# Kernel optimization log

Measured on AMD Instinct MI355X. Metric: run time of the kernel, lower is better.

Reference implementation:

```python
import jax, jax.numpy as jnp
import numpy as np
from jax.ops import segment_sum

N_NODES = 100000

def gcn_conv(x, ei, W, b, n):
    # PyG GCNConv: add self-loops, symmetric deg^-1/2 normalization,
    # linear transform (no lin bias), scatter-sum at target, then conv bias.
    src = jnp.concatenate([ei[0], jnp.arange(n)])  # [E+N]
    dst = jnp.concatenate([ei[1], jnp.arange(n)])
    deg = segment_sum(jnp.ones_like(dst, dtype=x.dtype), dst, num_segments=n)
    dinv = jnp.where(deg > 0, jax.lax.rsqrt(deg), 0.0)
    norm = dinv[src] * dinv[dst]                   # [E+N]
    h = x @ W.T                                    # [N, out] transform before gather
    msg = h[src] * norm[:, None]                   # [E+N, out]
    return segment_sum(msg, dst, num_segments=n) + b

def sage_conv_mean(x, ei, Wl, bl, Wr, n):
    # PyG SAGEConv(aggr='mean'): out = lin_l(mean_{j->i} x_j) + lin_r(x_i)
    src, dst = ei[0], ei[1]
    s = segment_sum(x[src], dst, num_segments=n)   # [N, d]
    cnt = segment_sum(jnp.ones_like(dst, dtype=x.dtype), dst, num_segments=n)
    mean = s / jnp.maximum(cnt, 1.0)[:, None]
    return mean @ Wl.T + bl + x @ Wr.T

def setup_inputs() -> dict:
    key = jax.random.key(0)
    k1, k2, k3, k4, k5, k6 = jax.random.split(key, 6)
    in_dim, hid = 128, 128
    n, e = N_NODES, 1600000
    feat = jax.random.normal(k1, (n, in_dim), dtype=jnp.float32)
    ei = jax.random.randint(k2, (2, e), 0, n, dtype=jnp.int64)
    W1 = jax.random.normal(k3, (hid, in_dim), dtype=jnp.float32) * 0.05
    b1 = jnp.zeros((hid,), dtype=jnp.float32)
    Wl = jax.random.normal(k4, (hid, hid), dtype=jnp.float32) * 0.05
    bl = jnp.zeros((hid,), dtype=jnp.float32)
    Wr = jax.random.normal(k5, (hid, hid), dtype=jnp.float32) * 0.05
    return {"feat": feat, "ei": ei, "W1": W1, "b1": b1, "Wl": Wl, "bl": bl, "Wr": Wr}

def reference(feat, ei, W1, b1, Wl, bl, Wr):
    n = feat.shape[0]
    h = jax.nn.relu(gcn_conv(feat, ei, W1, b1, n))
    h = jax.nn.relu(sage_conv_mean(h, ei, Wl, bl, Wr, n))
    return h
```

## Files before the change

### kernel.cpp

```cpp
#include <hip/hip_runtime.h>

typedef unsigned int uint;
typedef unsigned short ushort;
typedef short sv8 __attribute__((ext_vector_type(8)));
typedef float f32x4 __attribute__((ext_vector_type(4)));
typedef ushort u16x8 __attribute__((ext_vector_type(8)));

__device__ __forceinline__ ushort f2b(float f) {
  uint u = __float_as_uint(f);
  return (ushort)((u + 0x7FFFu + ((u >> 16) & 1u)) >> 16);
}
__device__ __forceinline__ float b2f_lo(uint p) { return __uint_as_float(p << 16); }
__device__ __forceinline__ float b2f_hi(uint p) { return __uint_as_float(p & 0xFFFF0000u); }
__device__ __forceinline__ uint cvtpk(float lo, float hi) {
  uint r;
  asm("v_cvt_pk_bf16_f32 %0, %1, %2" : "=v"(r) : "v"(lo), "v"(hi));
  return r;
}

#define MFMA16(acc, a, b) \
  asm volatile("v_mfma_f32_16x16x32_bf16 %0, %1, %2, %0" : "+v"(acc) : "v"(a), "v"(b))
#define DOT2(acc, p, d) \
  asm("v_dot2_f32_bf16 %0, %1, %2, %0" : "+v"(acc) : "v"(p), "v"(d))

#define GATHER16(SRC, jj)                                                     \
  {                                                                           \
    uint pa = (uint)__shfl((int)packed, (jj) + q);                            \
    uint pb = (uint)__shfl((int)packed, (jj) + 4 + q);                        \
    uint pc = (uint)__shfl((int)packed, (jj) + 8 + q);                        \
    uint pd = (uint)__shfl((int)packed, (jj) + 12 + q);                       \
    uint4 va = *(const uint4*)&SRC[(size_t)(pa & 0x1FFFFu) * 128 + lc * 8];   \
    uint4 vb = *(const uint4*)&SRC[(size_t)(pb & 0x1FFFFu) * 128 + lc * 8];   \
    uint4 vc = *(const uint4*)&SRC[(size_t)(pc & 0x1FFFFu) * 128 + lc * 8];   \
    uint4 vd = *(const uint4*)&SRC[(size_t)(pd & 0x1FFFFu) * 128 + lc * 8];   \
    uint dab = (pa >> 17) | ((pb >> 17) << 16);                               \
    uint dcd = (pc >> 17) | ((pd >> 17) << 16);                               \
    uint p;                                                                   \
    p = __builtin_amdgcn_perm(va.x, vb.x, 0x01000504u); DOT2(acc[0], p, dab); \
    p = __builtin_amdgcn_perm(va.x, vb.x, 0x03020706u); DOT2(acc[1], p, dab); \
    p = __builtin_amdgcn_perm(va.y, vb.y, 0x01000504u); DOT2(acc[2], p, dab); \
    p = __builtin_amdgcn_perm(va.y, vb.y, 0x03020706u); DOT2(acc[3], p, dab); \
    p = __builtin_amdgcn_perm(va.z, vb.z, 0x01000504u); DOT2(acc[4], p, dab); \
    p = __builtin_amdgcn_perm(va.z, vb.z, 0x03020706u); DOT2(acc[5], p, dab); \
    p = __builtin_amdgcn_perm(va.w, vb.w, 0x01000504u); DOT2(acc[6], p, dab); \
    p = __builtin_amdgcn_perm(va.w, vb.w, 0x03020706u); DOT2(acc[7], p, dab); \
    p = __builtin_amdgcn_perm(vc.x, vd.x, 0x01000504u); DOT2(acc[0], p, dcd); \
    p = __builtin_amdgcn_perm(vc.x, vd.x, 0x03020706u); DOT2(acc[1], p, dcd); \
    p = __builtin_amdgcn_perm(vc.y, vd.y, 0x01000504u); DOT2(acc[2], p, dcd); \
    p = __builtin_amdgcn_perm(vc.y, vd.y, 0x03020706u); DOT2(acc[3], p, dcd); \
    p = __builtin_amdgcn_perm(vc.z, vd.z, 0x01000504u); DOT2(acc[4], p, dcd); \
    p = __builtin_amdgcn_perm(vc.z, vd.z, 0x03020706u); DOT2(acc[5], p, dcd); \
    p = __builtin_amdgcn_perm(vc.w, vd.w, 0x01000504u); DOT2(acc[6], p, dcd); \
    p = __builtin_amdgcn_perm(vc.w, vd.w, 0x03020706u); DOT2(acc[7], p, dcd); \
  }


__global__ __launch_bounds__(256) void k_hist1(const int* __restrict__ dst,
                                               int* __restrict__ counts, int E) {
  __shared__ int h[256];
  int t = threadIdx.x;
  h[t] = 0;
  __syncthreads();
#pragma unroll
  for (int i = 0; i < 16; ++i) {
    int idx = blockIdx.x * 16384 + i * 1024 + t * 4;
    if (idx + 4 <= E) {
      int4 d = *(const int4*)&dst[idx];
      atomicAdd(&h[d.x >> 10], 1);
      atomicAdd(&h[d.y >> 10], 1);
      atomicAdd(&h[d.z >> 10], 1);
      atomicAdd(&h[d.w >> 10], 1);
    } else {
      for (int k = 0; k < 4; ++k)
        if (idx + k < E) atomicAdd(&h[dst[idx + k] >> 10], 1);
    }
  }
  __syncthreads();
  counts[blockIdx.x * 256 + t] = h[t];
}

__global__ __launch_bounds__(256) void k_colscan(int* __restrict__ counts,
                                                 int* __restrict__ bbase,
                                                 int* __restrict__ btot,
                                                 int* __restrict__ rowptr,
                                                 int NBLK, int N, int E) {
  __shared__ int s[256];
  int b = threadIdx.x;
  int run = 0;
#pragma unroll 4
  for (int blk = 0; blk < NBLK; ++blk) {
    int v = counts[blk * 256 + b];
    counts[blk * 256 + b] = run;
    run += v;
  }
  s[b] = run;
  __syncthreads();
  int incl = run;
  for (int off = 1; off < 256; off <<= 1) {
    int u = (b >= off) ? s[b - off] : 0;
    __syncthreads();
    s[b] += u;
    __syncthreads();
  }
  incl = s[b];
  bbase[b] = incl - run;
  btot[b] = run;
  if (b == 0) rowptr[N] = E;
}

__global__ __launch_bounds__(256) void k_scatter(const int* __restrict__ ei,
                                                 const int* __restrict__ counts,
                                                 const int* __restrict__ bbase,
                                                 uint* __restrict__ keyval, int E) {
  __shared__ int h[256];
  __shared__ int base[256];
  int t = threadIdx.x;
  base[t] = bbase[t] + counts[blockIdx.x * 256 + t];
  h[t] = 0;
  __syncthreads();
#pragma unroll
  for (int i = 0; i < 16; ++i) {
    int idx = blockIdx.x * 16384 + i * 1024 + t * 4;
    if (idx + 4 <= E) {
      int4 sv = *(const int4*)&ei[idx];
      int4 dv = *(const int4*)&ei[E + idx];
      int b0 = dv.x >> 10, b1 = dv.y >> 10, b2 = dv.z >> 10, b3 = dv.w >> 10;
      int r0 = atomicAdd(&h[b0], 1);
      keyval[base[b0] + r0] = (uint)sv.x | (((uint)dv.x & 1023u) << 17);
      int r1 = atomicAdd(&h[b1], 1);
      keyval[base[b1] + r1] = (uint)sv.y | (((uint)dv.y & 1023u) << 17);
      int r2 = atomicAdd(&h[b2], 1);
      keyval[base[b2] + r2] = (uint)sv.z | (((uint)dv.z & 1023u) << 17);
      int r3 = atomicAdd(&h[b3], 1);
      keyval[base[b3] + r3] = (uint)sv.w | (((uint)dv.w & 1023u) << 17);
    } else {
      for (int k = 0; k < 4; ++k)
        if (idx + k < E) {
          int sv = ei[idx + k], dv = ei[E + idx + k];
          int b = dv >> 10;
          int r = atomicAdd(&h[b], 1);
          keyval[base[b] + r] = (uint)sv | (((uint)dv & 1023u) << 17);
        }
    }
  }
}

__global__ __launch_bounds__(1024) void k_build(const uint* __restrict__ keyval,
                                                const int* __restrict__ bbase,
                                                const int* __restrict__ btot,
                                                int* __restrict__ rowptr,
                                                float* __restrict__ dinv,
                                                ushort* __restrict__ dinvb,
                                                int* __restrict__ col, int N) {
  __shared__ int c[1024];
  int b = blockIdx.x, t = threadIdx.x;
  int ebase = bbase[b], ecnt = btot[b];
  int node0 = b << 10;
  c[t] = 0;
  __syncthreads();
  for (int i = t; i < ecnt; i += 1024)
    atomicAdd(&c[keyval[ebase + i] >> 17], 1);
  __syncthreads();
  int v = c[t];
  for (int off = 1; off < 1024; off <<= 1) {
    int u = (t >= off) ? c[t - off] : 0;
    __syncthreads();
    c[t] += u;
    __syncthreads();
  }
  int excl = c[t] - v;
  int node = node0 + t;
  if (node < N) {
    float dv = rsqrtf((float)(v + 1));
    rowptr[node] = ebase + excl;
    dinv[node] = dv;
    dinvb[node] = f2b(dv);
  }
  __syncthreads();
  c[t] = excl;
  __syncthreads();
  for (int i = t; i < ecnt; i += 1024) {
    uint kv = keyval[ebase + i];
    int r = atomicAdd(&c[kv >> 17], 1);
    col[ebase + r] = (int)(kv & 0x1FFFFu);
  }
}


__global__ __launch_bounds__(256) void k_gemm1(const float* __restrict__ A,
                                               const float* __restrict__ W,
                                               ushort* __restrict__ Hb, int N) {
  __shared__ __align__(16) ushort smem[17408];
  int t = threadIdx.x;
#pragma unroll
  for (int i = 0; i < 8; ++i) {
    int c_ = t + i * 256;
    int row = c_ >> 4, slot = c_ & 15;
    const float* wp = &W[row * 128 + slot * 8];
    float4 w0 = *(const float4*)wp;
    float4 w1 = *(const float4*)(wp + 4);
    uint4 v = make_uint4(cvtpk(w0.x, w0.y), cvtpk(w0.z, w0.w),
                         cvtpk(w1.x, w1.y), cvtpk(w1.z, w1.w));
    *(uint4*)&smem[row * 128 + ((slot ^ (row & 7)) << 3)] = v;
  }
  __syncthreads();

  int wv = t >> 6, l = t & 63;
  int lr = l & 15, lk = l >> 4;
  int r0 = blockIdx.x * 256 + wv * 64;
  f32x4 acc[4][8];
#pragma unroll
  for (int rb = 0; rb < 4; ++rb)
#pragma unroll
    for (int ct = 0; ct < 8; ++ct) acc[rb][ct] = (f32x4){0.f, 0.f, 0.f, 0.f};

#pragma unroll
  for (int kk = 0; kk < 4; ++kk) {
    sv8 af[4];
#pragma unroll
    for (int rb = 0; rb < 4; ++rb) {
      int r = r0 + rb * 16 + lr;
      if (r >= N) r = N - 1;
      const float* ap = &A[(size_t)r * 128 + kk * 32 + lk * 8];
      float4 a0 = *(const float4*)ap;
      float4 a1 = *(const float4*)(ap + 4);
      uint4 au = make_uint4(cvtpk(a0.x, a0.y), cvtpk(a0.z, a0.w),
                            cvtpk(a1.x, a1.y), cvtpk(a1.z, a1.w));
      af[rb] = *(sv8*)&au;
    }
#pragma unroll
    for (int ct = 0; ct < 8; ++ct) {
      int brow = ct * 16 + lr;
      sv8 bf = *(const sv8*)&smem[brow * 128 + (((kk * 4 + lk) ^ (brow & 7)) << 3)];
      MFMA16(acc[0][ct], af[0], bf);
      MFMA16(acc[1][ct], af[1], bf);
      MFMA16(acc[2][ct], af[2], bf);
      MFMA16(acc[3][ct], af[3], bf);
    }
  }
  asm volatile("s_nop 7\n\ts_nop 7");
  __syncthreads();
  ushort* ep = smem + wv * (16 * 136);
#pragma unroll
  for (int rb = 0; rb < 4; ++rb) {
#pragma unroll
    for (int ct = 0; ct < 8; ++ct)
#pragma unroll
      for (int i = 0; i < 4; ++i)
        ep[(lk * 4 + i) * 136 + ct * 16 + lr] = f2b(acc[rb][ct][i]);
#pragma unroll
    for (int it = 0; it < 2; ++it) {
      int row = it * 8 + (l >> 3);
      int gr = r0 + rb * 16 + row;
      if (gr < N) {
#pragma unroll
        for (int cc = 0; cc < 2; ++cc) {
          int colv = cc * 64 + (l & 7) * 8;
          *(u16x8*)&Hb[(size_t)gr * 128 + colv] = *(const u16x8*)&ep[row * 136 + colv];
        }
      }
    }
  }
}


__global__ __launch_bounds__(256) void k_gemm2(const ushort* __restrict__ Mb,
                                               const ushort* __restrict__ X1b,
                                               const float* __restrict__ Wl,
                                               const float* __restrict__ Wr,
                                               const float* __restrict__ bl,
                                               float* __restrict__ Out, int N) {
  __shared__ __align__(16) ushort smem[2 * 128 * 128];
  int t = threadIdx.x;
#pragma unroll
  for (int i = 0; i < 8; ++i) {
    int c_ = t + i * 256;
    int row = c_ >> 4, slot = c_ & 15;
    int off = (slot ^ (row & 7)) << 3;
    {
      const float* wp = &Wl[row * 128 + slot * 8];
      float4 w0 = *(const float4*)wp;
      float4 w1 = *(const float4*)(wp + 4);
      *(uint4*)&smem[row * 128 + off] =
          make_uint4(cvtpk(w0.x, w0.y), cvtpk(w0.z, w0.w),
                     cvtpk(w1.x, w1.y), cvtpk(w1.z, w1.w));
    }
    {
      const float* wp = &Wr[row * 128 + slot * 8];
      float4 w0 = *(const float4*)wp;
      float4 w1 = *(const float4*)(wp + 4);
      *(uint4*)&smem[16384 + row * 128 + off] =
          make_uint4(cvtpk(w0.x, w0.y), cvtpk(w0.z, w0.w),
                     cvtpk(w1.x, w1.y), cvtpk(w1.z, w1.w));
    }
  }
  __syncthreads();

  int wv = t >> 6, l = t & 63;
  int lr = l & 15, lk = l >> 4;
  int r0 = blockIdx.x * 256 + wv * 64;
  f32x4 acc[4][8];
#pragma unroll
  for (int rb = 0; rb < 4; ++rb)
#pragma unroll
    for (int ct = 0; ct < 8; ++ct) acc[rb][ct] = (f32x4){0.f, 0.f, 0.f, 0.f};

#pragma unroll
  for (int ph = 0; ph < 2; ++ph) {
    const ushort* Ab = ph ? X1b : Mb;
    const ushort* Wp = smem + ph * 16384;
#pragma unroll
    for (int kk = 0; kk < 4; ++kk) {
      sv8 af[4];
#pragma unroll
      for (int rb = 0; rb < 4; ++rb) {
        int r = r0 + rb * 16 + lr;
        if (r >= N) r = N - 1;
        af[rb] = *(const sv8*)&Ab[(size_t)r * 128 + kk * 32 + lk * 8];
      }
#pragma unroll
      for (int ct = 0; ct < 8; ++ct) {
        int brow = ct * 16 + lr;
        sv8 bf = *(const sv8*)&Wp[brow * 128 + (((kk * 4 + lk) ^ (brow & 7)) << 3)];
        MFMA16(acc[0][ct], af[0], bf);
        MFMA16(acc[1][ct], af[1], bf);
        MFMA16(acc[2][ct], af[2], bf);
        MFMA16(acc[3][ct], af[3], bf);
      }
    }
  }
  asm volatile("s_nop 7\n\ts_nop 7");
  __syncthreads();
  float* epf = (float*)smem + wv * (16 * 132);
  float bb[8];
#pragma unroll
  for (int ct = 0; ct < 8; ++ct) bb[ct] = bl[ct * 16 + lr];
#pragma unroll
  for (int rb = 0; rb < 4; ++rb) {
#pragma unroll
    for (int ct = 0; ct < 8; ++ct)
#pragma unroll
      for (int i = 0; i < 4; ++i)
        epf[(lk * 4 + i) * 132 + ct * 16 + lr] = fmaxf(acc[rb][ct][i] + bb[ct], 0.f);
#pragma unroll
    for (int it = 0; it < 2; ++it) {
      int row = it * 8 + (l >> 3);
      int gr = r0 + rb * 16 + row;
      if (gr < N) {
#pragma unroll
        for (int cc = 0; cc < 4; ++cc) {
          int colv = cc * 32 + (l & 7) * 4;
          *(float4*)&Out[(size_t)gr * 128 + colv] = *(const float4*)&epf[row * 132 + colv];
        }
      }
    }
  }
}


__global__ __launch_bounds__(256) void k_agg_gcn(const ushort* __restrict__ Hb,
                                                 const int* __restrict__ rowptr,
                                                 const int* __restrict__ col,
                                                 const float* __restrict__ dinv,
                                                 const ushort* __restrict__ dinvb,
                                                 const float* __restrict__ bias,
                                                 ushort* __restrict__ X1b, int N) {
  int wid = (blockIdx.x * 256 + threadIdx.x) >> 6;
  int l = threadIdx.x & 63;
  if (wid >= N) return;
  int q = l >> 4, lc = l & 15;
  float di = dinv[wid];
  float acc[8] = {0.f, 0.f, 0.f, 0.f, 0.f, 0.f, 0.f, 0.f};
  int s0 = rowptr[wid], s1 = rowptr[wid + 1];
  for (int j0 = s0; j0 < s1; j0 += 64) {
    int rem = s1 - j0;
    uint packed = 0;
    if (l < rem) {
      int ix = col[j0 + l];
      packed = (uint)ix | ((uint)dinvb[ix] << 17);
    }
    int m = rem < 64 ? rem : 64;
    for (int jj = 0; jj < m; jj += 16) GATHER16(Hb, jj);
  }
#pragma unroll
  for (int k = 0; k < 8; ++k) {
    acc[k] += __shfl_xor(acc[k], 16);
    acc[k] += __shfl_xor(acc[k], 32);
  }
  if (q == 0) {
    uint4 hv = *(const uint4*)&Hb[(size_t)wid * 128 + lc * 8];
    float4 b0 = *(const float4*)&bias[lc * 8];
    float4 b1 = *(const float4*)&bias[lc * 8 + 4];
    float hvf[8] = {b2f_lo(hv.x), b2f_hi(hv.x), b2f_lo(hv.y), b2f_hi(hv.y),
                    b2f_lo(hv.z), b2f_hi(hv.z), b2f_lo(hv.w), b2f_hi(hv.w)};
    float bb[8] = {b0.x, b0.y, b0.z, b0.w, b1.x, b1.y, b1.z, b1.w};
    float o[8];
#pragma unroll
    for (int k = 0; k < 8; ++k)
      o[k] = fmaxf((acc[k] + hvf[k] * di) * di + bb[k], 0.f);
    uint4 r = make_uint4(cvtpk(o[0], o[1]), cvtpk(o[2], o[3]),
                         cvtpk(o[4], o[5]), cvtpk(o[6], o[7]));
    *(uint4*)&X1b[(size_t)wid * 128 + lc * 8] = r;
  }
}

__global__ __launch_bounds__(256) void k_agg_mean(const ushort* __restrict__ Xb,
                                                  const int* __restrict__ rowptr,
                                                  const int* __restrict__ col,
                                                  ushort* __restrict__ Mb, int N) {
  int wid = (blockIdx.x * 256 + threadIdx.x) >> 6;
  int l = threadIdx.x & 63;
  if (wid >= N) return;
  int q = l >> 4, lc = l & 15;
  float acc[8] = {0.f, 0.f, 0.f, 0.f, 0.f, 0.f, 0.f, 0.f};
  int s0 = rowptr[wid], s1 = rowptr[wid + 1];
  for (int j0 = s0; j0 < s1; j0 += 64) {
    int rem = s1 - j0;
    uint packed = 0;
    if (l < rem) packed = (uint)col[j0 + l] | (0x3F80u << 17);
    int m = rem < 64 ? rem : 64;
    for (int jj = 0; jj < m; jj += 16) GATHER16(Xb, jj);
  }
#pragma unroll
  for (int k = 0; k < 8; ++k) {
    acc[k] += __shfl_xor(acc[k], 16);
    acc[k] += __shfl_xor(acc[k], 32);
  }
  if (q == 0) {
    int deg = s1 - s0;
    float inv = 1.f / (float)(deg > 0 ? deg : 1);
    uint4 r = make_uint4(cvtpk(acc[0] * inv, acc[1] * inv),
                         cvtpk(acc[2] * inv, acc[3] * inv),
                         cvtpk(acc[4] * inv, acc[5] * inv),
                         cvtpk(acc[6] * inv, acc[7] * inv));
    *(uint4*)&Mb[(size_t)wid * 128 + lc * 8] = r;
  }
}


extern "C" void kernel_launch(void* const* d_in, const int* in_sizes, int n_in,
                              void* d_out, int out_size, void* d_ws, size_t ws_size,
                              hipStream_t stream) {
  const float* feat = (const float*)d_in[0];
  const int* ei     = (const int*)d_in[1];
  const float* W1   = (const float*)d_in[2];
  const float* b1   = (const float*)d_in[3];
  const float* Wl   = (const float*)d_in[4];
  const float* bl   = (const float*)d_in[5];
  const float* Wr   = (const float*)d_in[6];
  float* out = (float*)d_out;

  int N = in_sizes[0] / 128;
  int E = in_sizes[1] / 2;

  char* ws = (char*)d_ws;
  size_t off = 0;
  auto alloc = [&](size_t bytes) {
    void* p = ws + off;
    off += (bytes + 255) & ~(size_t)255;
    return p;
  };
  ushort* Hb    = (ushort*)alloc((size_t)N * 128 * 2);
  ushort* X1b   = (ushort*)alloc((size_t)N * 128 * 2);
  int*   rowptr = (int*)alloc((size_t)(N + 1) * 4);
  float* dinv   = (float*)alloc((size_t)N * 4);
  ushort* dinvb = (ushort*)alloc((size_t)N * 2);
  int*   col    = (int*)alloc((size_t)E * 4);
  int*   counts = (int*)alloc(128 * 256 * 4);
  int*   bbase  = (int*)alloc(1024);
  int*   btot   = (int*)alloc(1024);
  uint* keyval = (uint*)Hb;

  int NB = (N + 1023) >> 10;
  int NBLK = (E + 16383) / 16384;

  k_hist1<<<NBLK, 256, 0, stream>>>(ei + E, counts, E);
  k_colscan<<<1, 256, 0, stream>>>(counts, bbase, btot, rowptr, NBLK, N, E);
  k_scatter<<<NBLK, 256, 0, stream>>>(ei, counts, bbase, keyval, E);
  k_build<<<NB, 1024, 0, stream>>>(keyval, bbase, btot, rowptr, dinv, dinvb, col, N);

  int gb = (N + 255) / 256;
  k_gemm1<<<gb, 256, 0, stream>>>(feat, W1, Hb, N);
  k_agg_gcn<<<(N + 3) / 4, 256, 0, stream>>>(Hb, rowptr, col, dinv, dinvb, b1, X1b, N);
  k_agg_mean<<<(N + 3) / 4, 256, 0, stream>>>(X1b, rowptr, col, Hb, N);
  k_gemm2<<<gb, 256, 0, stream>>>(Hb, X1b, Wl, Wr, bl, out, N);
}
```

Measured before the change: 206.9 us.

## Split neighbor aggregation across feature slices with more waves per node

```diff
diff --git a/kernel.cpp b/kernel.cpp
--- a/kernel.cpp
+++ b/kernel.cpp
@@ -20,39 +20,6 @@
 
 #define MFMA16(acc, a, b) \
   asm volatile("v_mfma_f32_16x16x32_bf16 %0, %1, %2, %0" : "+v"(acc) : "v"(a), "v"(b))
-#define DOT2(acc, p, d) \
-  asm("v_dot2_f32_bf16 %0, %1, %2, %0" : "+v"(acc) : "v"(p), "v"(d))
-
-#define GATHER16(SRC, jj)                                                     \
-  {                                                                           \
-    uint pa = (uint)__shfl((int)packed, (jj) + q);                            \
-    uint pb = (uint)__shfl((int)packed, (jj) + 4 + q);                        \
-    uint pc = (uint)__shfl((int)packed, (jj) + 8 + q);                        \
-    uint pd = (uint)__shfl((int)packed, (jj) + 12 + q);                       \
-    uint4 va = *(const uint4*)&SRC[(size_t)(pa & 0x1FFFFu) * 128 + lc * 8];   \
-    uint4 vb = *(const uint4*)&SRC[(size_t)(pb & 0x1FFFFu) * 128 + lc * 8];   \
-    uint4 vc = *(const uint4*)&SRC[(size_t)(pc & 0x1FFFFu) * 128 + lc * 8];   \
-    uint4 vd = *(const uint4*)&SRC[(size_t)(pd & 0x1FFFFu) * 128 + lc * 8];   \
-    uint dab = (pa >> 17) | ((pb >> 17) << 16);                               \
-    uint dcd = (pc >> 17) | ((pd >> 17) << 16);                               \
-    uint p;                                                                   \
-    p = __builtin_amdgcn_perm(va.x, vb.x, 0x01000504u); DOT2(acc[0], p, dab); \
-    p = __builtin_amdgcn_perm(va.x, vb.x, 0x03020706u); DOT2(acc[1], p, dab); \
-    p = __builtin_amdgcn_perm(va.y, vb.y, 0x01000504u); DOT2(acc[2], p, dab); \
-    p = __builtin_amdgcn_perm(va.y, vb.y, 0x03020706u); DOT2(acc[3], p, dab); \
-    p = __builtin_amdgcn_perm(va.z, vb.z, 0x01000504u); DOT2(acc[4], p, dab); \
-    p = __builtin_amdgcn_perm(va.z, vb.z, 0x03020706u); DOT2(acc[5], p, dab); \
-    p = __builtin_amdgcn_perm(va.w, vb.w, 0x01000504u); DOT2(acc[6], p, dab); \
-    p = __builtin_amdgcn_perm(va.w, vb.w, 0x03020706u); DOT2(acc[7], p, dab); \
-    p = __builtin_amdgcn_perm(vc.x, vd.x, 0x01000504u); DOT2(acc[0], p, dcd); \
-    p = __builtin_amdgcn_perm(vc.x, vd.x, 0x03020706u); DOT2(acc[1], p, dcd); \
-    p = __builtin_amdgcn_perm(vc.y, vd.y, 0x01000504u); DOT2(acc[2], p, dcd); \
-    p = __builtin_amdgcn_perm(vc.y, vd.y, 0x03020706u); DOT2(acc[3], p, dcd); \
-    p = __builtin_amdgcn_perm(vc.z, vd.z, 0x01000504u); DOT2(acc[4], p, dcd); \
-    p = __builtin_amdgcn_perm(vc.z, vd.z, 0x03020706u); DOT2(acc[5], p, dcd); \
-    p = __builtin_amdgcn_perm(vc.w, vd.w, 0x01000504u); DOT2(acc[6], p, dcd); \
-    p = __builtin_amdgcn_perm(vc.w, vd.w, 0x03020706u); DOT2(acc[7], p, dcd); \
-  }
 
 
 __global__ __launch_bounds__(256) void k_hist1(const int* __restrict__ dst,
@@ -95,15 +62,13 @@
   }
   s[b] = run;
   __syncthreads();
-  int incl = run;
   for (int off = 1; off < 256; off <<= 1) {
     int u = (b >= off) ? s[b - off] : 0;
     __syncthreads();
     s[b] += u;
     __syncthreads();
   }
-  incl = s[b];
-  bbase[b] = incl - run;
+  bbase[b] = s[b] - run;
   btot[b] = run;
   if (b == 0) rowptr[N] = E;
 }
@@ -358,39 +323,65 @@
 }
 
 
-__global__ __launch_bounds__(256) void k_agg_gcn(const ushort* __restrict__ Hb,
-                                                 const int* __restrict__ rowptr,
-                                                 const int* __restrict__ col,
-                                                 const float* __restrict__ dinv,
-                                                 const ushort* __restrict__ dinvb,
-                                                 const float* __restrict__ bias,
-                                                 ushort* __restrict__ X1b, int N) {
-  int wid = (blockIdx.x * 256 + threadIdx.x) >> 6;
+#define AGG_SLICE_LOOP(SRC)                                                   \
+  for (int j0 = s0; j0 < s1; j0 += 64) {                                      \
+    int rem = s1 - j0;                                                        \
+    uint packed = 0;                                                          \
+    if (l < rem) {                                                            \
+      int ix = col[j0 + l];                                                   \
+      packed = (uint)ix | (WEIGHT(ix) << 17);                                 \
+    }                                                                         \
+    int m = rem < 64 ? rem : 64;                                              \
+    for (int jj = 0; jj < m; jj += 32) {                                      \
+      int r = jj + q2;                                                        \
+      uint pa = (uint)__shfl((int)packed, r);       \
+      if (r < m) {                                                            \
+        float wa = __uint_as_float((pa >> 17) << 16);                         \
+        uint4 v = *(const uint4*)&SRC[(size_t)(pa & 0x1FFFFu) * 128];         \
+        acc[0] = fmaf(b2f_lo(v.x), wa, acc[0]);                               \
+        acc[1] = fmaf(b2f_hi(v.x), wa, acc[1]);                               \
+        acc[2] = fmaf(b2f_lo(v.y), wa, acc[2]);                               \
+        acc[3] = fmaf(b2f_hi(v.y), wa, acc[3]);                               \
+        acc[4] = fmaf(b2f_lo(v.z), wa, acc[4]);                               \
+        acc[5] = fmaf(b2f_hi(v.z), wa, acc[5]);                               \
+        acc[6] = fmaf(b2f_lo(v.w), wa, acc[6]);                               \
+        acc[7] = fmaf(b2f_hi(v.w), wa, acc[7]);                               \
+      }                                                                       \
+    }                                                                         \
+  }                                                                           \
+  _Pragma("unroll")                                                           \
+  for (int k = 0; k < 8; ++k) {                                               \
+    acc[k] += __shfl_xor(acc[k], 2);                                          \
+    acc[k] += __shfl_xor(acc[k], 4);                                          \
+    acc[k] += __shfl_xor(acc[k], 8);                                          \
+    acc[k] += __shfl_xor(acc[k], 16);                                         \
+    acc[k] += __shfl_xor(acc[k], 32);                                         \
+  }
+
+__global__ __launch_bounds__(512) void k_agg_gcn_s(const ushort* __restrict__ Hb,
+                                                   const int* __restrict__ rowptr,
+                                                   const int* __restrict__ col,
+                                                   const float* __restrict__ dinv,
+                                                   const ushort* __restrict__ dinvb,
+                                                   const float* __restrict__ bias,
+                                                   ushort* __restrict__ X1b, int N) {
+  int slice = blockIdx.x & 7;
+  int wid = (blockIdx.x >> 3) * 8 + (threadIdx.x >> 6);
   int l = threadIdx.x & 63;
   if (wid >= N) return;
-  int q = l >> 4, lc = l & 15;
-  float di = dinv[wid];
+  int q2 = l >> 1, lc2 = l & 1;
+  int fo = slice * 16 + lc2 * 8;
+  const ushort* Hs = Hb + fo;
   float acc[8] = {0.f, 0.f, 0.f, 0.f, 0.f, 0.f, 0.f, 0.f};
   int s0 = rowptr[wid], s1 = rowptr[wid + 1];
-  for (int j0 = s0; j0 < s1; j0 += 64) {
-    int rem = s1 - j0;
-    uint packed = 0;
-    if (l < rem) {
-      int ix = col[j0 + l];
-      packed = (uint)ix | ((uint)dinvb[ix] << 17);
-    }
-    int m = rem < 64 ? rem : 64;
-    for (int jj = 0; jj < m; jj += 16) GATHER16(Hb, jj);
-  }
-#pragma unroll
-  for (int k = 0; k < 8; ++k) {
-    acc[k] += __shfl_xor(acc[k], 16);
-    acc[k] += __shfl_xor(acc[k], 32);
-  }
-  if (q == 0) {
-    uint4 hv = *(const uint4*)&Hb[(size_t)wid * 128 + lc * 8];
-    float4 b0 = *(const float4*)&bias[lc * 8];
-    float4 b1 = *(const float4*)&bias[lc * 8 + 4];
+#define WEIGHT(ix) ((uint)dinvb[ix])
+  AGG_SLICE_LOOP(Hs)
+#undef WEIGHT
+  if (q2 == 0) {
+    float di = dinv[wid];
+    uint4 hv = *(const uint4*)&Hs[(size_t)wid * 128];
+    float4 b0 = *(const float4*)&bias[fo];
+    float4 b1 = *(const float4*)&bias[fo + 4];
     float hvf[8] = {b2f_lo(hv.x), b2f_hi(hv.x), b2f_lo(hv.y), b2f_hi(hv.y),
                     b2f_lo(hv.z), b2f_hi(hv.z), b2f_lo(hv.w), b2f_hi(hv.w)};
     float bb[8] = {b0.x, b0.y, b0.z, b0.w, b1.x, b1.y, b1.z, b1.w};
@@ -400,40 +391,34 @@
       o[k] = fmaxf((acc[k] + hvf[k] * di) * di + bb[k], 0.f);
     uint4 r = make_uint4(cvtpk(o[0], o[1]), cvtpk(o[2], o[3]),
                          cvtpk(o[4], o[5]), cvtpk(o[6], o[7]));
-    *(uint4*)&X1b[(size_t)wid * 128 + lc * 8] = r;
-  }
-}
-
-__global__ __launch_bounds__(256) void k_agg_mean(const ushort* __restrict__ Xb,
-                                                  const int* __restrict__ rowptr,
-                                                  const int* __restrict__ col,
-                                                  ushort* __restrict__ Mb, int N) {
-  int wid = (blockIdx.x * 256 + threadIdx.x) >> 6;
+    *(uint4*)&X1b[(size_t)wid * 128 + fo] = r;
+  }
+}
+
+__global__ __launch_bounds__(512) void k_agg_mean_s(const ushort* __restrict__ Xb,
+                                                    const int* __restrict__ rowptr,
+                                                    const int* __restrict__ col,
+                                                    ushort* __restrict__ Mb, int N) {
+  int slice = blockIdx.x & 7;
+  int wid = (blockIdx.x >> 3) * 8 + (threadIdx.x >> 6);
   int l = threadIdx.x & 63;
   if (wid >= N) return;
-  int q = l >> 4, lc = l & 15;
+  int q2 = l >> 1, lc2 = l & 1;
+  int fo = slice * 16 + lc2 * 8;
+  const ushort* Xs = Xb + fo;
   float acc[8] = {0.f, 0.f, 0.f, 0.f, 0.f, 0.f, 0.f, 0.f};
   int s0 = rowptr[wid], s1 = rowptr[wid + 1];
-  for (int j0 = s0; j0 < s1; j0 += 64) {
-    int rem = s1 - j0;
-    uint packed = 0;
-    if (l < rem) packed = (uint)col[j0 + l] | (0x3F80u << 17);
-    int m = rem < 64 ? rem : 64;
-    for (int jj = 0; jj < m; jj += 16) GATHER16(Xb, jj);
-  }
-#pragma unroll
-  for (int k = 0; k < 8; ++k) {
-    acc[k] += __shfl_xor(acc[k], 16);
-    acc[k] += __shfl_xor(acc[k], 32);
-  }
-  if (q == 0) {
+#define WEIGHT(ix) (0x3F80u)
+  AGG_SLICE_LOOP(Xs)
+#undef WEIGHT
+  if (q2 == 0) {
     int deg = s1 - s0;
     float inv = 1.f / (float)(deg > 0 ? deg : 1);
     uint4 r = make_uint4(cvtpk(acc[0] * inv, acc[1] * inv),
                          cvtpk(acc[2] * inv, acc[3] * inv),
                          cvtpk(acc[4] * inv, acc[5] * inv),
                          cvtpk(acc[6] * inv, acc[7] * inv));
-    *(uint4*)&Mb[(size_t)wid * 128 + lc * 8] = r;
+    *(uint4*)&Mb[(size_t)wid * 128 + fo] = r;
   }
 }
 
@@ -480,8 +465,9 @@
   k_build<<<NB, 1024, 0, stream>>>(keyval, bbase, btot, rowptr, dinv, dinvb, col, N);
 
   int gb = (N + 255) / 256;
+  int ab = ((N + 7) / 8) * 8;
   k_gemm1<<<gb, 256, 0, stream>>>(feat, W1, Hb, N);
-  k_agg_gcn<<<(N + 3) / 4, 256, 0, stream>>>(Hb, rowptr, col, dinv, dinvb, b1, X1b, N);
-  k_agg_mean<<<(N + 3) / 4, 256, 0, stream>>>(X1b, rowptr, col, Hb, N);
+  k_agg_gcn_s<<<ab, 512, 0, stream>>>(Hb, rowptr, col, dinv, dinvb, b1, X1b, N);
+  k_agg_mean_s<<<ab, 512, 0, stream>>>(X1b, rowptr, col, Hb, N);
   k_gemm2<<<gb, 256, 0, stream>>>(Hb, X1b, Wl, Wr, bl, out, N);
 }
```

New measurement: 765.0 us. +269.7%, slower.
